# Optimization experiments

Measured on AMD Instinct MI355X. Metric: run time of the kernel, lower is better.

## Reference

```python
import jax, jax.numpy as jnp
import numpy as np

N_EXPERTS = 8
D_MODEL = 1024
D_FF = 4096


def setup_inputs() -> dict:
    key = jax.random.key(0)
    k_x, k_idx, k_g, k_u, k_d = jax.random.split(key, 5)
    scale_in = 1.0 / np.sqrt(D_MODEL)
    scale_ff = 1.0 / np.sqrt(D_FF)
    return {
        "x": jax.random.normal(k_x, (2, 1024, D_MODEL), dtype=jnp.float32),
        "expert_idx": jax.random.randint(k_idx, (2, 1024), 0, N_EXPERTS, dtype=jnp.int64),
        "w_gate": jax.random.normal(k_g, (N_EXPERTS, D_MODEL, D_FF), dtype=jnp.float32) * scale_in,
        "w_up": jax.random.normal(k_u, (N_EXPERTS, D_MODEL, D_FF), dtype=jnp.float32) * scale_in,
        "w_down": jax.random.normal(k_d, (N_EXPERTS, D_FF, D_MODEL), dtype=jnp.float32) * scale_ff,
    }


def reference(x, expert_idx, w_gate, w_up, w_down):
    # x: [B, S, D]; expert_idx: [B, S] in [0, N_EXPERTS)
    B, S, D = x.shape
    x_flat = x.reshape(-1, D)                  # [T, D]
    idx_flat = expert_idx.reshape(-1)          # [T]
    out = jnp.zeros_like(x_flat)
    # Faithful per-expert dispatch: each token is processed by exactly one
    # expert's SwiGLU FFN; masked scatter-back combines results.
    for e in range(N_EXPERTS):
        mask = (idx_flat == e)[:, None]        # [T, 1]
        gate = jax.nn.silu(x_flat @ w_gate[e]) # [T, F]
        up = x_flat @ w_up[e]                  # [T, F]
        y = (gate * up) @ w_down[e]            # [T, D]
        out = jnp.where(mask, y, out)
    return out.reshape(B, S, D)
```

## Files before the change

### kernel.cpp

```cpp
#include <hip/hip_runtime.h>
#include <hip/hip_bf16.h>
#include <stdint.h>

#define N_EXPERTS 8
#define D_MODEL   1024
#define D_FF      4096
#define T_TOKENS  2048
#define MT        256
#define MAXT      16
#define KSPLIT    8
#define BK        64
#define KP        72

typedef __attribute__((ext_vector_type(8))) short bf16x8;
typedef __attribute__((ext_vector_type(4))) float f32x4;

__device__ __forceinline__ short f2bf(float f) {
    union { float f; uint32_t u; } v; v.f = f;
    uint32_t u = v.u;
    return (short)((u + 0x7fffu + ((u >> 16) & 1u)) >> 16);
}

__device__ __forceinline__ uint32_t pack2bf(float a, float b) {
    __hip_bfloat162 h = __float22bfloat162_rn(make_float2(a, b));
    return *(uint32_t*)&h;
}

template<int STRIDE>
__device__ __forceinline__ void ldw16(float v[16], const float* __restrict__ src) {
#pragma unroll
    for (int j = 0; j < 16; ++j) v[j] = src[(size_t)j * STRIDE];
}

__device__ __forceinline__ void stw16(short* dst, const float v[16]) {
    uint4 w0, w1;
    w0.x = pack2bf(v[0], v[1]);  w0.y = pack2bf(v[2], v[3]);
    w0.z = pack2bf(v[4], v[5]);  w0.w = pack2bf(v[6], v[7]);
    w1.x = pack2bf(v[8], v[9]);  w1.y = pack2bf(v[10], v[11]);
    w1.z = pack2bf(v[12], v[13]); w1.w = pack2bf(v[14], v[15]);
    *(uint4*)dst = w0;
    *(uint4*)(dst + 8) = w1;
}


__global__ void moe_route(const int* __restrict__ idx, int* __restrict__ offsets,
                          int* __restrict__ ntp, int* __restrict__ t_e,
                          int* __restrict__ t_p0, int* __restrict__ t_end) {
    __shared__ int cnt[N_EXPERTS];
    int tid = threadIdx.x;
    if (tid < N_EXPERTS) cnt[tid] = 0;
    __syncthreads();
    for (int t = tid; t < T_TOKENS; t += 256) atomicAdd(&cnt[idx[t]], 1);
    __syncthreads();
    if (tid == 0) {
        int off = 0, nt = 0;
        for (int e = 0; e < N_EXPERTS; ++e) {
            offsets[e] = off;
            int c = cnt[e], end = off + c;
            for (int i = 0; i < c; i += MT) { t_e[nt] = e; t_p0[nt] = off + i; t_end[nt] = end; ++nt; }
            off = end;
        }
        offsets[N_EXPERTS] = off;
        *ntp = nt;
    }
}

__global__ void moe_gather(const float* __restrict__ x, const int* __restrict__ idx,
                           const int* __restrict__ offsets, int* __restrict__ cursor,
                           int* __restrict__ tok_of_row, short* __restrict__ Xg) {
    __shared__ int sp;
    int t = blockIdx.x;
    if (threadIdx.x == 0) {
        int e = idx[t];
        int p = offsets[e] + atomicAdd(&cursor[e], 1);
        tok_of_row[p] = t;
        sp = p;
    }
    __syncthreads();
    int p = sp;
    const float4* src = (const float4*)(x + (size_t)t * D_MODEL);
    uint2* dst = (uint2*)(Xg + (size_t)p * D_MODEL);
    int i = threadIdx.x;
    float4 v = src[i];
    uint2 o;
    o.x = pack2bf(v.x, v.y);
    o.y = pack2bf(v.z, v.w);
    dst[i] = o;
}


__launch_bounds__(256, 2)
__global__ void moe_gemm1(const float* __restrict__ wg, const float* __restrict__ wu,
                          const short* __restrict__ Xg, short* __restrict__ h,
                          const int* __restrict__ t_e, const int* __restrict__ t_p0,
                          const int* __restrict__ t_end, const int* __restrict__ ntp) {
    int ti = blockIdx.y;
    if (ti >= *ntp) return;
    int e = t_e[ti], p0 = t_p0[ti], pend = t_end[ti];
    int n0 = blockIdx.x * 64;

    __shared__ short Bg[2][64][KP];
    __shared__ short Bu[2][64][KP];

    int tid = threadIdx.x;
    int nl = tid & 63, kc = tid >> 6;
    int lane = tid & 63, w = tid >> 6;
    int col = lane & 15, quad = lane >> 4;

    const float* wgb = wg + (size_t)e * D_MODEL * D_FF + (size_t)(kc * 16) * D_FF + n0 + nl;
    const float* wub = wu + (size_t)e * D_MODEL * D_FF + (size_t)(kc * 16) * D_FF + n0 + nl;

    const short* ap[4];
#pragma unroll
    for (int m = 0; m < 4; ++m) {
        int r = p0 + w * 64 + m * 16 + col;
        if (r > T_TOKENS - 1) r = T_TOKENS - 1;
        ap[m] = Xg + (size_t)r * D_MODEL + quad * 8;
    }

    f32x4 accg[4][4], accu[4][4];
#pragma unroll
    for (int m = 0; m < 4; ++m)
#pragma unroll
        for (int nf = 0; nf < 4; ++nf) {
            accg[m][nf] = (f32x4){0,0,0,0};
            accu[m][nf] = (f32x4){0,0,0,0};
        }

    {
        float g0[16], u0[16];
        ldw16<D_FF>(g0, wgb);
        ldw16<D_FF>(u0, wub);
        stw16(&Bg[0][nl][kc * 16], g0);
        stw16(&Bu[0][nl][kc * 16], u0);
    }
    __syncthreads();

    const int NIT = D_MODEL / BK;
    int p = 0;
#pragma unroll 1
    for (int it = 0; it < NIT; ++it) {
        int kn = (it + 1 == NIT) ? 0 : (it + 1) * BK;
        float gn[16], un[16];
        ldw16<D_FF>(gn, wgb + (size_t)kn * D_FF);
        ldw16<D_FF>(un, wub + (size_t)kn * D_FF);
        int kb = it * BK;

#pragma unroll
        for (int ks = 0; ks < 2; ++ks) {
            bf16x8 a0 = *(const bf16x8*)(ap[0] + kb + ks * 32);
            bf16x8 a1 = *(const bf16x8*)(ap[1] + kb + ks * 32);
            bf16x8 a2 = *(const bf16x8*)(ap[2] + kb + ks * 32);
            bf16x8 a3 = *(const bf16x8*)(ap[3] + kb + ks * 32);
#pragma unroll
            for (int nf = 0; nf < 4; ++nf) {
                bf16x8 bg = *(const bf16x8*)&Bg[p][nf * 16 + col][ks * 32 + quad * 8];
                bf16x8 bu = *(const bf16x8*)&Bu[p][nf * 16 + col][ks * 32 + quad * 8];
                accg[0][nf] = __builtin_amdgcn_mfma_f32_16x16x32_bf16(a0, bg, accg[0][nf], 0, 0, 0);
                accg[1][nf] = __builtin_amdgcn_mfma_f32_16x16x32_bf16(a1, bg, accg[1][nf], 0, 0, 0);
                accg[2][nf] = __builtin_amdgcn_mfma_f32_16x16x32_bf16(a2, bg, accg[2][nf], 0, 0, 0);
                accg[3][nf] = __builtin_amdgcn_mfma_f32_16x16x32_bf16(a3, bg, accg[3][nf], 0, 0, 0);
                accu[0][nf] = __builtin_amdgcn_mfma_f32_16x16x32_bf16(a0, bu, accu[0][nf], 0, 0, 0);
                accu[1][nf] = __builtin_amdgcn_mfma_f32_16x16x32_bf16(a1, bu, accu[1][nf], 0, 0, 0);
                accu[2][nf] = __builtin_amdgcn_mfma_f32_16x16x32_bf16(a2, bu, accu[2][nf], 0, 0, 0);
                accu[3][nf] = __builtin_amdgcn_mfma_f32_16x16x32_bf16(a3, bu, accu[3][nf], 0, 0, 0);
            }
        }

        stw16(&Bg[p ^ 1][nl][kc * 16], gn);
        stw16(&Bu[p ^ 1][nl][kc * 16], un);
        __syncthreads();
        p ^= 1;
    }

#pragma unroll
    for (int m = 0; m < 4; ++m) {
#pragma unroll
        for (int r = 0; r < 4; ++r) {
            int mr = p0 + w * 64 + m * 16 + quad * 4 + r;
            if (mr < pend) {
#pragma unroll
                for (int nf = 0; nf < 4; ++nf) {
                    float gv = accg[m][nf][r], uv = accu[m][nf][r];
                    float hv = (gv / (1.f + __expf(-gv))) * uv;
                    h[(size_t)mr * D_FF + n0 + nf * 16 + col] = f2bf(hv);
                }
            }
        }
    }
}


__launch_bounds__(256, 3)
__global__ void moe_gemm2(const float* __restrict__ wd, const short* __restrict__ h,
                          const int* __restrict__ tok_of_row, float* __restrict__ out,
                          const int* __restrict__ t_e, const int* __restrict__ t_p0,
                          const int* __restrict__ t_end, const int* __restrict__ ntp) {
    int ti = blockIdx.y;
    if (ti >= *ntp) return;
    int e = t_e[ti], p0 = t_p0[ti], pend = t_end[ti];
    int d0 = blockIdx.x * 64;
    int Koff = blockIdx.z * (D_FF / KSPLIT);

    __shared__ short Bd[2][64][KP];

    int tid = threadIdx.x;
    int nl = tid & 63, kc = tid >> 6;
    int lane = tid & 63, w = tid >> 6;
    int col = lane & 15, quad = lane >> 4;

    const float* wb = wd + (size_t)e * D_FF * D_MODEL + (size_t)(Koff + kc * 16) * D_MODEL + d0 + nl;

    const short* ap[4];
#pragma unroll
    for (int m = 0; m < 4; ++m) {
        int r = p0 + w * 64 + m * 16 + col;
        if (r > T_TOKENS - 1) r = T_TOKENS - 1;
        ap[m] = h + (size_t)r * D_FF + Koff + quad * 8;
    }

    f32x4 acc[4][4];
#pragma unroll
    for (int m = 0; m < 4; ++m)
#pragma unroll
        for (int nf = 0; nf < 4; ++nf) acc[m][nf] = (f32x4){0,0,0,0};

    {
        float w0[16];
        ldw16<D_MODEL>(w0, wb);
        stw16(&Bd[0][nl][kc * 16], w0);
    }
    __syncthreads();

    const int NIT = (D_FF / KSPLIT) / BK;
    int p = 0;
#pragma unroll 1
    for (int it = 0; it < NIT; ++it) {
        int kn = (it + 1 == NIT) ? 0 : (it + 1) * BK;
        float wn[16];
        ldw16<D_MODEL>(wn, wb + (size_t)kn * D_MODEL);
        int kb = it * BK;

#pragma unroll
        for (int ks = 0; ks < 2; ++ks) {
            bf16x8 a0 = *(const bf16x8*)(ap[0] + kb + ks * 32);
            bf16x8 a1 = *(const bf16x8*)(ap[1] + kb + ks * 32);
            bf16x8 a2 = *(const bf16x8*)(ap[2] + kb + ks * 32);
            bf16x8 a3 = *(const bf16x8*)(ap[3] + kb + ks * 32);
#pragma unroll
            for (int nf = 0; nf < 4; ++nf) {
                bf16x8 b = *(const bf16x8*)&Bd[p][nf * 16 + col][ks * 32 + quad * 8];
                acc[0][nf] = __builtin_amdgcn_mfma_f32_16x16x32_bf16(a0, b, acc[0][nf], 0, 0, 0);
                acc[1][nf] = __builtin_amdgcn_mfma_f32_16x16x32_bf16(a1, b, acc[1][nf], 0, 0, 0);
                acc[2][nf] = __builtin_amdgcn_mfma_f32_16x16x32_bf16(a2, b, acc[2][nf], 0, 0, 0);
                acc[3][nf] = __builtin_amdgcn_mfma_f32_16x16x32_bf16(a3, b, acc[3][nf], 0, 0, 0);
            }
        }

        stw16(&Bd[p ^ 1][nl][kc * 16], wn);
        __syncthreads();
        p ^= 1;
    }

#pragma unroll
    for (int m = 0; m < 4; ++m) {
#pragma unroll
        for (int r = 0; r < 4; ++r) {
            int mr = p0 + w * 64 + m * 16 + quad * 4 + r;
            if (mr < pend) {
                int t = tok_of_row[mr];
#pragma unroll
                for (int nf = 0; nf < 4; ++nf)
                    atomicAdd(&out[(size_t)t * D_MODEL + d0 + nf * 16 + col], acc[m][nf][r]);
            }
        }
    }
}


extern "C" void kernel_launch(void* const* d_in, const int* in_sizes, int n_in,
                              void* d_out, int out_size, void* d_ws, size_t ws_size,
                              hipStream_t stream) {
    (void)in_sizes; (void)n_in; (void)out_size; (void)ws_size;
    const float* x   = (const float*)d_in[0];
    const int*   idx = (const int*)d_in[1];
    const float* wg  = (const float*)d_in[2];
    const float* wu  = (const float*)d_in[3];
    const float* wd  = (const float*)d_in[4];
    float* out = (float*)d_out;

    int* ws_i       = (int*)d_ws;
    int* cursor     = ws_i;
    int* offsets    = ws_i + 8;
    int* nt         = ws_i + 20;
    int* t_e        = ws_i + 32;
    int* t_p0       = ws_i + 48;
    int* t_end      = ws_i + 64;
    int* tok_of_row = ws_i + 256;

    short* Xg = (short*)((char*)d_ws + 16384);
    short* h  = (short*)((char*)d_ws + 16384 + (size_t)T_TOKENS * D_MODEL * 2);

    hipMemsetAsync(d_ws, 0, 128, stream);
    hipMemsetAsync(out, 0, (size_t)T_TOKENS * D_MODEL * sizeof(float), stream);
    moe_route<<<dim3(1), 256, 0, stream>>>(idx, offsets, nt, t_e, t_p0, t_end);
    moe_gather<<<dim3(T_TOKENS), 256, 0, stream>>>(x, idx, offsets, cursor, tok_of_row, Xg);
    moe_gemm1<<<dim3(D_FF / 64, MAXT), 256, 0, stream>>>(wg, wu, Xg, h,
                                                         t_e, t_p0, t_end, nt);
    moe_gemm2<<<dim3(D_MODEL / 64, MAXT, KSPLIT), 256, 0, stream>>>(wd, h, tok_of_row, out,
                                                                    t_e, t_p0, t_end, nt);
}
```

Before: 559.6 us.

## Pre-repack weights to swizzled bf16 tiles and stream via global_load_lds

```diff
diff --git a/kernel.cpp b/kernel.cpp
--- a/kernel.cpp
+++ b/kernel.cpp
@@ -6,40 +6,36 @@
 #define D_MODEL   1024
 #define D_FF      4096
 #define T_TOKENS  2048
-#define MT        256
-#define MAXT      16
-#define KSPLIT    8
-#define BK        64
-#define KP        72
+#define MT        128
+#define MAXT      24
+#define KSPLIT    4
 
 typedef __attribute__((ext_vector_type(8))) short bf16x8;
 typedef __attribute__((ext_vector_type(4))) float f32x4;
 
-__device__ __forceinline__ short f2bf(float f) {
+#define XG_OFF   (16384)
+#define H_OFF    (16384 + 4u*1024*1024)
+#define WG_OFF   (32u*1024*1024)
+#define WU_OFF   (96u*1024*1024)
+#define WD_OFF   (160u*1024*1024)
+
+__device__ __forceinline__ unsigned short f2bfu(float f) {
     union { float f; uint32_t u; } v; v.f = f;
     uint32_t u = v.u;
-    return (short)((u + 0x7fffu + ((u >> 16) & 1u)) >> 16);
-}
+    return (unsigned short)((u + 0x7fffu + ((u >> 16) & 1u)) >> 16);
+}
+
+__device__ __forceinline__ short f2bf(float f) { return (short)f2bfu(f); }
 
 __device__ __forceinline__ uint32_t pack2bf(float a, float b) {
     __hip_bfloat162 h = __float22bfloat162_rn(make_float2(a, b));
     return *(uint32_t*)&h;
 }
 
-template<int STRIDE>
-__device__ __forceinline__ void ldw16(float v[16], const float* __restrict__ src) {
-#pragma unroll
-    for (int j = 0; j < 16; ++j) v[j] = src[(size_t)j * STRIDE];
-}
-
-__device__ __forceinline__ void stw16(short* dst, const float v[16]) {
-    uint4 w0, w1;
-    w0.x = pack2bf(v[0], v[1]);  w0.y = pack2bf(v[2], v[3]);
-    w0.z = pack2bf(v[4], v[5]);  w0.w = pack2bf(v[6], v[7]);
-    w1.x = pack2bf(v[8], v[9]);  w1.y = pack2bf(v[10], v[11]);
-    w1.z = pack2bf(v[12], v[13]); w1.w = pack2bf(v[14], v[15]);
-    *(uint4*)dst = w0;
-    *(uint4*)(dst + 8) = w1;
+__device__ __forceinline__ void gl_lds16(const short* g, short* l) {
+    __builtin_amdgcn_global_load_lds(
+        (const __attribute__((address_space(1))) unsigned int*)(g),
+        (__attribute__((address_space(3))) unsigned int*)(l), 16, 0, 0);
 }
 
 
@@ -89,101 +85,162 @@
 }
 
 
-__launch_bounds__(256, 2)
-__global__ void moe_gemm1(const float* __restrict__ wg, const float* __restrict__ wu,
+__launch_bounds__(256)
+__global__ void moe_repack(const float* __restrict__ src, short* __restrict__ dst,
+                           int K, int N) {
+    __shared__ short Lt[256][72];
+
+    int e = blockIdx.z, kslab = blockIdx.y, nslab = blockIdx.x;
+    int NT = N >> 6, KS = K >> 6;
+    int tid = threadIdx.x;
+    int w = tid >> 6, l = tid & 63;
+
+    const float* sb = src + ((size_t)e * K + (size_t)kslab * 64) * N
+                      + (size_t)nslab * 256 + 4 * l;
+
+#pragma unroll
+    for (int g = 0; g < 4; ++g) {
+        int r0 = g * 16 + w * 4;
+        float4 v0 = *(const float4*)(sb + (size_t)(r0    ) * N);
+        float4 v1 = *(const float4*)(sb + (size_t)(r0 + 1) * N);
+        float4 v2 = *(const float4*)(sb + (size_t)(r0 + 2) * N);
+        float4 v3 = *(const float4*)(sb + (size_t)(r0 + 3) * N);
+        {
+            int n = 4 * l + 0; int cc = r0 ^ (((n >> 3) & 3) << 3);
+            ushort4 tv = { f2bfu(v0.x), f2bfu(v1.x), f2bfu(v2.x), f2bfu(v3.x) };
+            *(ushort4*)&Lt[n][cc] = tv;
+        }
+        {
+            int n = 4 * l + 1; int cc = r0 ^ (((n >> 3) & 3) << 3);
+            ushort4 tv = { f2bfu(v0.y), f2bfu(v1.y), f2bfu(v2.y), f2bfu(v3.y) };
+            *(ushort4*)&Lt[n][cc] = tv;
+        }
+        {
+            int n = 4 * l + 2; int cc = r0 ^ (((n >> 3) & 3) << 3);
+            ushort4 tv = { f2bfu(v0.z), f2bfu(v1.z), f2bfu(v2.z), f2bfu(v3.z) };
+            *(ushort4*)&Lt[n][cc] = tv;
+        }
+        {
+            int n = 4 * l + 3; int cc = r0 ^ (((n >> 3) & 3) << 3);
+            ushort4 tv = { f2bfu(v0.w), f2bfu(v1.w), f2bfu(v2.w), f2bfu(v3.w) };
+            *(ushort4*)&Lt[n][cc] = tv;
+        }
+    }
+    __syncthreads();
+
+    int t = tid >> 6, idx = tid & 63;
+#pragma unroll
+    for (int i = 0; i < 8; ++i) {
+        int u = i * 64 + idx;
+        int n = u >> 3, k8 = u & 7;
+        int sw = ((n >> 3) & 3) << 3;
+        bf16x8 vv = *(const bf16x8*)&Lt[t * 64 + n][(k8 * 8) ^ sw];
+        size_t tb = (((size_t)e * NT + (size_t)nslab * 4 + t) * KS + kslab) * 4096;
+        *(bf16x8*)&dst[tb + n * 64 + ((k8 ^ (n & 7)) * 8)] = vv;
+    }
+}
+
+
+__launch_bounds__(256)
+__global__ void moe_gemm1(const short* __restrict__ wgt, const short* __restrict__ wut,
                           const short* __restrict__ Xg, short* __restrict__ h,
                           const int* __restrict__ t_e, const int* __restrict__ t_p0,
                           const int* __restrict__ t_end, const int* __restrict__ ntp) {
     int ti = blockIdx.y;
     if (ti >= *ntp) return;
     int e = t_e[ti], p0 = t_p0[ti], pend = t_end[ti];
-    int n0 = blockIdx.x * 64;
-
-    __shared__ short Bg[2][64][KP];
-    __shared__ short Bu[2][64][KP];
+    int nt = blockIdx.x;
+
+    __shared__ short Bg[2][4096];
+    __shared__ short Bu[2][4096];
 
     int tid = threadIdx.x;
-    int nl = tid & 63, kc = tid >> 6;
     int lane = tid & 63, w = tid >> 6;
     int col = lane & 15, quad = lane >> 4;
 
-    const float* wgb = wg + (size_t)e * D_MODEL * D_FF + (size_t)(kc * 16) * D_FF + n0 + nl;
-    const float* wub = wu + (size_t)e * D_MODEL * D_FF + (size_t)(kc * 16) * D_FF + n0 + nl;
-
-    const short* ap[4];
-#pragma unroll
-    for (int m = 0; m < 4; ++m) {
-        int r = p0 + w * 64 + m * 16 + col;
-        if (r > T_TOKENS - 1) r = T_TOKENS - 1;
-        ap[m] = Xg + (size_t)r * D_MODEL + quad * 8;
-    }
-
-    f32x4 accg[4][4], accu[4][4];
-#pragma unroll
-    for (int m = 0; m < 4; ++m)
+    const short* gsrc = wgt + ((size_t)e * 64 + nt) * 16 * 4096 + w * 1024 + lane * 8;
+    const short* usrc = wut + ((size_t)e * 64 + nt) * 16 * 4096 + w * 1024 + lane * 8;
+
+    int row0 = p0 + w * 32 + col;  if (row0 > T_TOKENS - 1) row0 = T_TOKENS - 1;
+    int row1 = row0 + 16;          if (row1 > T_TOKENS - 1) row1 = T_TOKENS - 1;
+    const short* a0p = Xg + (size_t)row0 * D_MODEL + quad * 8;
+    const short* a1p = Xg + (size_t)row1 * D_MODEL + quad * 8;
+
+    int boff0[4], boff1[4];
+#pragma unroll
+    for (int nf = 0; nf < 4; ++nf) {
+        int n = nf * 16 + col;
+        boff0[nf] = n * 64 + ((quad ^ (n & 7)) * 8);
+        boff1[nf] = n * 64 + (((quad + 4) ^ (n & 7)) * 8);
+    }
+
+    f32x4 accg[2][4], accu[2][4];
+#pragma unroll
+    for (int m = 0; m < 2; ++m)
 #pragma unroll
         for (int nf = 0; nf < 4; ++nf) {
             accg[m][nf] = (f32x4){0,0,0,0};
             accu[m][nf] = (f32x4){0,0,0,0};
         }
 
-    {
-        float g0[16], u0[16];
-        ldw16<D_FF>(g0, wgb);
-        ldw16<D_FF>(u0, wub);
-        stw16(&Bg[0][nl][kc * 16], g0);
-        stw16(&Bu[0][nl][kc * 16], u0);
-    }
-    __syncthreads();
-
-    const int NIT = D_MODEL / BK;
+    gl_lds16(gsrc,       &Bg[0][w * 1024]);
+    gl_lds16(gsrc + 512, &Bg[0][w * 1024 + 512]);
+    gl_lds16(usrc,       &Bu[0][w * 1024]);
+    gl_lds16(usrc + 512, &Bu[0][w * 1024 + 512]);
+    bf16x8 a00 = *(const bf16x8*)(a0p);
+    bf16x8 a01 = *(const bf16x8*)(a0p + 32);
+    bf16x8 a10 = *(const bf16x8*)(a1p);
+    bf16x8 a11 = *(const bf16x8*)(a1p + 32);
+    __syncthreads();
+
     int p = 0;
 #pragma unroll 1
-    for (int it = 0; it < NIT; ++it) {
-        int kn = (it + 1 == NIT) ? 0 : (it + 1) * BK;
-        float gn[16], un[16];
-        ldw16<D_FF>(gn, wgb + (size_t)kn * D_FF);
-        ldw16<D_FF>(un, wub + (size_t)kn * D_FF);
-        int kb = it * BK;
-
-#pragma unroll
-        for (int ks = 0; ks < 2; ++ks) {
-            bf16x8 a0 = *(const bf16x8*)(ap[0] + kb + ks * 32);
-            bf16x8 a1 = *(const bf16x8*)(ap[1] + kb + ks * 32);
-            bf16x8 a2 = *(const bf16x8*)(ap[2] + kb + ks * 32);
-            bf16x8 a3 = *(const bf16x8*)(ap[3] + kb + ks * 32);
-#pragma unroll
-            for (int nf = 0; nf < 4; ++nf) {
-                bf16x8 bg = *(const bf16x8*)&Bg[p][nf * 16 + col][ks * 32 + quad * 8];
-                bf16x8 bu = *(const bf16x8*)&Bu[p][nf * 16 + col][ks * 32 + quad * 8];
-                accg[0][nf] = __builtin_amdgcn_mfma_f32_16x16x32_bf16(a0, bg, accg[0][nf], 0, 0, 0);
-                accg[1][nf] = __builtin_amdgcn_mfma_f32_16x16x32_bf16(a1, bg, accg[1][nf], 0, 0, 0);
-                accg[2][nf] = __builtin_amdgcn_mfma_f32_16x16x32_bf16(a2, bg, accg[2][nf], 0, 0, 0);
-                accg[3][nf] = __builtin_amdgcn_mfma_f32_16x16x32_bf16(a3, bg, accg[3][nf], 0, 0, 0);
-                accu[0][nf] = __builtin_amdgcn_mfma_f32_16x16x32_bf16(a0, bu, accu[0][nf], 0, 0, 0);
-                accu[1][nf] = __builtin_amdgcn_mfma_f32_16x16x32_bf16(a1, bu, accu[1][nf], 0, 0, 0);
-                accu[2][nf] = __builtin_amdgcn_mfma_f32_16x16x32_bf16(a2, bu, accu[2][nf], 0, 0, 0);
-                accu[3][nf] = __builtin_amdgcn_mfma_f32_16x16x32_bf16(a3, bu, accu[3][nf], 0, 0, 0);
-            }
-        }
-
-        stw16(&Bg[p ^ 1][nl][kc * 16], gn);
-        stw16(&Bu[p ^ 1][nl][kc * 16], un);
+    for (int it = 0; it < 16; ++it) {
+        int itn = (it + 1) & 15;
+        const short* gs = gsrc + (size_t)itn * 4096;
+        const short* us = usrc + (size_t)itn * 4096;
+        gl_lds16(gs,       &Bg[p ^ 1][w * 1024]);
+        gl_lds16(gs + 512, &Bg[p ^ 1][w * 1024 + 512]);
+        gl_lds16(us,       &Bu[p ^ 1][w * 1024]);
+        gl_lds16(us + 512, &Bu[p ^ 1][w * 1024 + 512]);
+        int kn = itn * 64;
+        bf16x8 a00n = *(const bf16x8*)(a0p + kn);
+        bf16x8 a01n = *(const bf16x8*)(a0p + kn + 32);
+        bf16x8 a10n = *(const bf16x8*)(a1p + kn);
+        bf16x8 a11n = *(const bf16x8*)(a1p + kn + 32);
+
+#pragma unroll
+        for (int nf = 0; nf < 4; ++nf) {
+            bf16x8 bg0 = *(const bf16x8*)&Bg[p][boff0[nf]];
+            bf16x8 bg1 = *(const bf16x8*)&Bg[p][boff1[nf]];
+            bf16x8 bu0 = *(const bf16x8*)&Bu[p][boff0[nf]];
+            bf16x8 bu1 = *(const bf16x8*)&Bu[p][boff1[nf]];
+            accg[0][nf] = __builtin_amdgcn_mfma_f32_16x16x32_bf16(a00, bg0, accg[0][nf], 0, 0, 0);
+            accg[0][nf] = __builtin_amdgcn_mfma_f32_16x16x32_bf16(a01, bg1, accg[0][nf], 0, 0, 0);
+            accg[1][nf] = __builtin_amdgcn_mfma_f32_16x16x32_bf16(a10, bg0, accg[1][nf], 0, 0, 0);
+            accg[1][nf] = __builtin_amdgcn_mfma_f32_16x16x32_bf16(a11, bg1, accg[1][nf], 0, 0, 0);
+            accu[0][nf] = __builtin_amdgcn_mfma_f32_16x16x32_bf16(a00, bu0, accu[0][nf], 0, 0, 0);
+            accu[0][nf] = __builtin_amdgcn_mfma_f32_16x16x32_bf16(a01, bu1, accu[0][nf], 0, 0, 0);
+            accu[1][nf] = __builtin_amdgcn_mfma_f32_16x16x32_bf16(a10, bu0, accu[1][nf], 0, 0, 0);
+            accu[1][nf] = __builtin_amdgcn_mfma_f32_16x16x32_bf16(a11, bu1, accu[1][nf], 0, 0, 0);
+        }
+
+        a00 = a00n; a01 = a01n; a10 = a10n; a11 = a11n;
         __syncthreads();
         p ^= 1;
     }
 
 #pragma unroll
-    for (int m = 0; m < 4; ++m) {
+    for (int m = 0; m < 2; ++m) {
 #pragma unroll
         for (int r = 0; r < 4; ++r) {
-            int mr = p0 + w * 64 + m * 16 + quad * 4 + r;
+            int mr = p0 + w * 32 + m * 16 + quad * 4 + r;
             if (mr < pend) {
 #pragma unroll
                 for (int nf = 0; nf < 4; ++nf) {
                     float gv = accg[m][nf][r], uv = accu[m][nf][r];
                     float hv = (gv / (1.f + __expf(-gv))) * uv;
-                    h[(size_t)mr * D_FF + n0 + nf * 16 + col] = f2bf(hv);
+                    h[(size_t)mr * D_FF + nt * 64 + nf * 16 + col] = f2bf(hv);
                 }
             }
         }
@@ -191,87 +248,90 @@
 }
 
 
-__launch_bounds__(256, 3)
-__global__ void moe_gemm2(const float* __restrict__ wd, const short* __restrict__ h,
+__launch_bounds__(256)
+__global__ void moe_gemm2(const short* __restrict__ wdt, const short* __restrict__ h,
                           const int* __restrict__ tok_of_row, float* __restrict__ out,
                           const int* __restrict__ t_e, const int* __restrict__ t_p0,
                           const int* __restrict__ t_end, const int* __restrict__ ntp) {
     int ti = blockIdx.y;
     if (ti >= *ntp) return;
     int e = t_e[ti], p0 = t_p0[ti], pend = t_end[ti];
-    int d0 = blockIdx.x * 64;
-    int Koff = blockIdx.z * (D_FF / KSPLIT);
-
-    __shared__ short Bd[2][64][KP];
+    int dt = blockIdx.x, z = blockIdx.z;
+
+    __shared__ short Bd[2][4096];
 
     int tid = threadIdx.x;
-    int nl = tid & 63, kc = tid >> 6;
     int lane = tid & 63, w = tid >> 6;
     int col = lane & 15, quad = lane >> 4;
 
-    const float* wb = wd + (size_t)e * D_FF * D_MODEL + (size_t)(Koff + kc * 16) * D_MODEL + d0 + nl;
-
-    const short* ap[4];
-#pragma unroll
-    for (int m = 0; m < 4; ++m) {
-        int r = p0 + w * 64 + m * 16 + col;
-        if (r > T_TOKENS - 1) r = T_TOKENS - 1;
-        ap[m] = h + (size_t)r * D_FF + Koff + quad * 8;
-    }
-
-    f32x4 acc[4][4];
-#pragma unroll
-    for (int m = 0; m < 4; ++m)
+    const short* dsrc = wdt + (((size_t)e * 16 + dt) * 64 + z * 16) * 4096 + w * 1024 + lane * 8;
+    int Koff = z * (D_FF / KSPLIT);
+
+    int row0 = p0 + w * 32 + col;  if (row0 > T_TOKENS - 1) row0 = T_TOKENS - 1;
+    int row1 = row0 + 16;          if (row1 > T_TOKENS - 1) row1 = T_TOKENS - 1;
+    const short* a0p = h + (size_t)row0 * D_FF + Koff + quad * 8;
+    const short* a1p = h + (size_t)row1 * D_FF + Koff + quad * 8;
+
+    int boff0[4], boff1[4];
+#pragma unroll
+    for (int nf = 0; nf < 4; ++nf) {
+        int n = nf * 16 + col;
+        boff0[nf] = n * 64 + ((quad ^ (n & 7)) * 8);
+        boff1[nf] = n * 64 + (((quad + 4) ^ (n & 7)) * 8);
+    }
+
+    f32x4 acc[2][4];
+#pragma unroll
+    for (int m = 0; m < 2; ++m)
 #pragma unroll
         for (int nf = 0; nf < 4; ++nf) acc[m][nf] = (f32x4){0,0,0,0};
 
-    {
-        float w0[16];
-        ldw16<D_MODEL>(w0, wb);
-        stw16(&Bd[0][nl][kc * 16], w0);
-    }
-    __syncthreads();
-
-    const int NIT = (D_FF / KSPLIT) / BK;
+    gl_lds16(dsrc,       &Bd[0][w * 1024]);
+    gl_lds16(dsrc + 512, &Bd[0][w * 1024 + 512]);
+    bf16x8 a00 = *(const bf16x8*)(a0p);
+    bf16x8 a01 = *(const bf16x8*)(a0p + 32);
+    bf16x8 a10 = *(const bf16x8*)(a1p);
+    bf16x8 a11 = *(const bf16x8*)(a1p + 32);
+    __syncthreads();
+
     int p = 0;
 #pragma unroll 1
-    for (int it = 0; it < NIT; ++it) {
-        int kn = (it + 1 == NIT) ? 0 : (it + 1) * BK;
-        float wn[16];
-        ldw16<D_MODEL>(wn, wb + (size_t)kn * D_MODEL);
-        int kb = it * BK;
-
-#pragma unroll
-        for (int ks = 0; ks < 2; ++ks) {
-            bf16x8 a0 = *(const bf16x8*)(ap[0] + kb + ks * 32);
-            bf16x8 a1 = *(const bf16x8*)(ap[1] + kb + ks * 32);
-            bf16x8 a2 = *(const bf16x8*)(ap[2] + kb + ks * 32);
-            bf16x8 a3 = *(const bf16x8*)(ap[3] + kb + ks * 32);
-#pragma unroll
-            for (int nf = 0; nf < 4; ++nf) {
-                bf16x8 b = *(const bf16x8*)&Bd[p][nf * 16 + col][ks * 32 + quad * 8];
-                acc[0][nf] = __builtin_amdgcn_mfma_f32_16x16x32_bf16(a0, b, acc[0][nf], 0, 0, 0);
-                acc[1][nf] = __builtin_amdgcn_mfma_f32_16x16x32_bf16(a1, b, acc[1][nf], 0, 0, 0);
-                acc[2][nf] = __builtin_amdgcn_mfma_f32_16x16x32_bf16(a2, b, acc[2][nf], 0, 0, 0);
-                acc[3][nf] = __builtin_amdgcn_mfma_f32_16x16x32_bf16(a3, b, acc[3][nf], 0, 0, 0);
-            }
-        }
-
-        stw16(&Bd[p ^ 1][nl][kc * 16], wn);
+    for (int it = 0; it < 16; ++it) {
+        int itn = (it + 1) & 15;
+        const short* ds = dsrc + (size_t)itn * 4096;
+        gl_lds16(ds,       &Bd[p ^ 1][w * 1024]);
+        gl_lds16(ds + 512, &Bd[p ^ 1][w * 1024 + 512]);
+        int kn = itn * 64;
+        bf16x8 a00n = *(const bf16x8*)(a0p + kn);
+        bf16x8 a01n = *(const bf16x8*)(a0p + kn + 32);
+        bf16x8 a10n = *(const bf16x8*)(a1p + kn);
+        bf16x8 a11n = *(const bf16x8*)(a1p + kn + 32);
+
+#pragma unroll
+        for (int nf = 0; nf < 4; ++nf) {
+            bf16x8 b0 = *(const bf16x8*)&Bd[p][boff0[nf]];
+            bf16x8 b1 = *(const bf16x8*)&Bd[p][boff1[nf]];
+            acc[0][nf] = __builtin_amdgcn_mfma_f32_16x16x32_bf16(a00, b0, acc[0][nf], 0, 0, 0);
+            acc[0][nf] = __builtin_amdgcn_mfma_f32_16x16x32_bf16(a01, b1, acc[0][nf], 0, 0, 0);
+            acc[1][nf] = __builtin_amdgcn_mfma_f32_16x16x32_bf16(a10, b0, acc[1][nf], 0, 0, 0);
+            acc[1][nf] = __builtin_amdgcn_mfma_f32_16x16x32_bf16(a11, b1, acc[1][nf], 0, 0, 0);
+        }
+
+        a00 = a00n; a01 = a01n; a10 = a10n; a11 = a11n;
         __syncthreads();
         p ^= 1;
     }
 
 #pragma unroll
-    for (int m = 0; m < 4; ++m) {
+    for (int m = 0; m < 2; ++m) {
 #pragma unroll
         for (int r = 0; r < 4; ++r) {
-            int mr = p0 + w * 64 + m * 16 + quad * 4 + r;
+            int mr = p0 + w * 32 + m * 16 + quad * 4 + r;
             if (mr < pend) {
                 int t = tok_of_row[mr];
 #pragma unroll
                 for (int nf = 0; nf < 4; ++nf)
-                    atomicAdd(&out[(size_t)t * D_MODEL + d0 + nf * 16 + col], acc[m][nf][r]);
+                    atomicAdd(&out[(size_t)t * D_MODEL + dt * 64 + nf * 16 + col], acc[m][nf][r]);
             }
         }
     }
@@ -294,19 +354,25 @@
     int* offsets    = ws_i + 8;
     int* nt         = ws_i + 20;
     int* t_e        = ws_i + 32;
-    int* t_p0       = ws_i + 48;
-    int* t_end      = ws_i + 64;
+    int* t_p0       = ws_i + 64;
+    int* t_end      = ws_i + 96;
     int* tok_of_row = ws_i + 256;
 
-    short* Xg = (short*)((char*)d_ws + 16384);
-    short* h  = (short*)((char*)d_ws + 16384 + (size_t)T_TOKENS * D_MODEL * 2);
+    short* Xg  = (short*)((char*)d_ws + XG_OFF);
+    short* h   = (short*)((char*)d_ws + H_OFF);
+    short* WGt = (short*)((char*)d_ws + WG_OFF);
+    short* WUt = (short*)((char*)d_ws + WU_OFF);
+    short* WDt = (short*)((char*)d_ws + WD_OFF);
 
     hipMemsetAsync(d_ws, 0, 128, stream);
     hipMemsetAsync(out, 0, (size_t)T_TOKENS * D_MODEL * sizeof(float), stream);
     moe_route<<<dim3(1), 256, 0, stream>>>(idx, offsets, nt, t_e, t_p0, t_end);
     moe_gather<<<dim3(T_TOKENS), 256, 0, stream>>>(x, idx, offsets, cursor, tok_of_row, Xg);
-    moe_gemm1<<<dim3(D_FF / 64, MAXT), 256, 0, stream>>>(wg, wu, Xg, h,
+    moe_repack<<<dim3(D_FF / 256, D_MODEL / 64, N_EXPERTS), 256, 0, stream>>>(wg, WGt, D_MODEL, D_FF);
+    moe_repack<<<dim3(D_FF / 256, D_MODEL / 64, N_EXPERTS), 256, 0, stream>>>(wu, WUt, D_MODEL, D_FF);
+    moe_repack<<<dim3(D_MODEL / 256, D_FF / 64, N_EXPERTS), 256, 0, stream>>>(wd, WDt, D_FF, D_MODEL);
+    moe_gemm1<<<dim3(D_FF / 64, MAXT), 256, 0, stream>>>(WGt, WUt, Xg, h,
                                                          t_e, t_p0, t_end, nt);
-    moe_gemm2<<<dim3(D_MODEL / 64, MAXT, KSPLIT), 256, 0, stream>>>(wd, h, tok_of_row, out,
+    moe_gemm2<<<dim3(D_MODEL / 64, MAXT, KSPLIT), 256, 0, stream>>>(WDt, h, tok_of_row, out,
                                                                     t_e, t_p0, t_end, nt);
 }
```

Result: slower. 605.5 us (+8.2%).
